# Optimization experiments

Hardware: AMD Instinct MI355X
Metric: run time of the kernel (lower is better)

## Reference

```python
import jax, jax.numpy as jnp
import numpy as np

SIZE = 4096       # reservoir width
STEPS = 512       # num_steps
BETA = 1.0        # leak factor (LSMNeuron default beta=1.0)
THRESHOLD = 10.0  # LSMNeuron threshold=10

# Heaviside spike with atan surrogate gradient (snntorch default surrogate)
@jax.custom_vjp
def heaviside(x):
    return (x > 0).astype(x.dtype)

def _h_fwd(x):
    return (x > 0).astype(x.dtype), x

def _h_bwd(x, g):
    # snntorch ATan surrogate with alpha=2: d/dx = 1 / (1 + (pi*x)^2)
    return (g / (1.0 + (jnp.pi * x) ** 2),)

heaviside.defvjp(_h_fwd, _h_bwd)


def setup_inputs() -> dict:
    key = jax.random.key(0)
    kx, kw = jax.random.split(key)
    x = jax.random.normal(kx, (STEPS, SIZE), dtype=jnp.float32)
    # fc1 weight: Linear(2*size, size), no bias. Input half | recurrent half.
    W = jax.random.normal(kw, (SIZE, 2 * SIZE), dtype=jnp.float32) / np.sqrt(2 * SIZE)
    return {"x": x, "W": W}


def reference(x, W):
    # Split weight: Wx acts on the external input, Ws on recurrent spikes.
    Wx = W[:, :SIZE]   # [size, size]
    Ws = W[:, SIZE:]   # [size, size]
    # Precompute the input-driven current for all steps as one big GEMM.
    cur_x = jnp.einsum('ts,os->to', x, Wx)  # [steps, size]

    def step(carry, cur_xt):
        spk, mem = carry
        cur = cur_xt + Ws @ spk            # fc1(concat(x[t], spk))
        mem = BETA * mem + cur             # leaky integrate
        spk = heaviside(mem - THRESHOLD)   # fire
        mem = mem - spk * THRESHOLD        # subtract reset
        return (spk, mem), (spk, mem)

    init = (jnp.zeros((SIZE,), jnp.float32), jnp.zeros((SIZE,), jnp.float32))
    _, (spk_rec, mem_rec) = jax.lax.scan(step, init, cur_x)
    # original detaches spk_rec
    return jax.lax.stop_gradient(spk_rec), mem_rec
```

## Files before the change

kernel.cpp:

```cpp
#include <hip/hip_runtime.h>
#include <stdint.h>

#define N_SIZE 4096
#define N_STEPS 512
#define WROW 8192
#define THRESH 10.0f
#define CCAP 12

#define WST_BYTES ((size_t)(N_SIZE + 1) * N_SIZE * 4)
#define SMEM_OFF  WST_BYTES
#define SLST_OFF  (WST_BYTES + (size_t)N_SIZE * 4)
#define FULL_WS   (SLST_OFF + (size_t)(N_SIZE + 17) * 4)

#define F4E(v, j) ((j) == 0 ? (v).x : (j) == 1 ? (v).y : (j) == 2 ? (v).z : (v).w)
#define ADD4(a, b) { (a).x += (b).x; (a).y += (b).y; (a).z += (b).z; (a).w += (b).w; }

__global__ __launch_bounds__(256) void k_transpose(const float* __restrict__ W,
                                                   float* __restrict__ WsT) {
    __shared__ float tile[32][33];
    const int bs = blockIdx.x * 32;
    const int bo = blockIdx.y * 32;
    const int tx = threadIdx.x;
    const int ty = threadIdx.y;
#pragma unroll
    for (int j = 0; j < 4; ++j)
        tile[ty + j * 8][tx] = W[(size_t)(bo + ty + j * 8) * WROW + N_SIZE + bs + tx];
    __syncthreads();
#pragma unroll
    for (int j = 0; j < 4; ++j)
        WsT[(size_t)(bs + ty + j * 8) * N_SIZE + bo + tx] = tile[tx][ty + j * 8];
}

__global__ __launch_bounds__(256) void k_zero_row(float* __restrict__ WsT) {
    WsT[(size_t)N_SIZE * N_SIZE + blockIdx.x * 256 + threadIdx.x] = 0.f;
}

#define BM 64
#define BN 128
#define BK 16
#define KHALF (N_SIZE / 2)
#define ALD 68
#define BLD 132

__global__ __launch_bounds__(128) void k_gemm(const float* __restrict__ x,
                                              const float* __restrict__ W,
                                              float* __restrict__ dst0,
                                              float* __restrict__ dst1) {
    __shared__ float As[BK][ALD];
    __shared__ float Bs[BK][BLD];
    const int tid = threadIdx.x;
    const int bm = blockIdx.y * BM;
    const int bn = blockIdx.x * BN;
    const int kb0 = blockIdx.z * KHALF;
    float* dst = blockIdx.z ? dst1 : dst0;

    const int m0 = (tid >> 4) << 3;
    const int n0 = (tid & 15) << 2;
    const int ar = tid >> 2;
    const int ac = (tid & 3) << 2;
    const float* Ap = &x[(size_t)(bm + ar) * N_SIZE + kb0 + ac];
    const float* Bp = &W[(size_t)(bn + ar) * WROW + kb0 + ac];

    float4 pa0 = *(const float4*)&Ap[0];
    float4 pa1 = *(const float4*)&Ap[(size_t)32 * N_SIZE];
    float4 pb0 = *(const float4*)&Bp[0];
    float4 pb1 = *(const float4*)&Bp[(size_t)32 * WROW];
    float4 pb2 = *(const float4*)&Bp[(size_t)64 * WROW];
    float4 pb3 = *(const float4*)&Bp[(size_t)96 * WROW];

    float acc[8][8];
#pragma unroll
    for (int i = 0; i < 8; ++i)
#pragma unroll
        for (int j = 0; j < 8; ++j) acc[i][j] = 0.f;

    const int nkt = KHALF / BK;
    for (int kt = 0; kt < nkt; ++kt) {
        __syncthreads();
#pragma unroll
        for (int j = 0; j < 4; ++j) {
            As[ac + j][ar]      = F4E(pa0, j);
            As[ac + j][ar + 32] = F4E(pa1, j);
            Bs[ac + j][ar]      = F4E(pb0, j);
            Bs[ac + j][ar + 32] = F4E(pb1, j);
            Bs[ac + j][ar + 64] = F4E(pb2, j);
            Bs[ac + j][ar + 96] = F4E(pb3, j);
        }
        __syncthreads();
        if (kt + 1 < nkt) {
            const float* Ap2 = Ap + (size_t)(kt + 1) * BK;
            const float* Bp2 = Bp + (size_t)(kt + 1) * BK;
            pa0 = *(const float4*)&Ap2[0];
            pa1 = *(const float4*)&Ap2[(size_t)32 * N_SIZE];
            pb0 = *(const float4*)&Bp2[0];
            pb1 = *(const float4*)&Bp2[(size_t)32 * WROW];
            pb2 = *(const float4*)&Bp2[(size_t)64 * WROW];
            pb3 = *(const float4*)&Bp2[(size_t)96 * WROW];
        }
#pragma unroll
        for (int k = 0; k < BK; ++k) {
            const float4 a0 = *(const float4*)&As[k][m0];
            const float4 a1 = *(const float4*)&As[k][m0 + 4];
            const float4 b0 = *(const float4*)&Bs[k][n0];
            const float4 b1 = *(const float4*)&Bs[k][n0 + 64];
            const float av[8] = {a0.x, a0.y, a0.z, a0.w, a1.x, a1.y, a1.z, a1.w};
            const float bv[8] = {b0.x, b0.y, b0.z, b0.w, b1.x, b1.y, b1.z, b1.w};
#pragma unroll
            for (int i = 0; i < 8; ++i)
#pragma unroll
                for (int j = 0; j < 8; ++j)
                    acc[i][j] = fmaf(av[i], bv[j], acc[i][j]);
        }
    }
#pragma unroll
    for (int i = 0; i < 8; ++i) {
        float* cp = &dst[(size_t)(bm + m0 + i) * N_SIZE + bn];
        const float4 o0 = {acc[i][0], acc[i][1], acc[i][2], acc[i][3]};
        const float4 o1 = {acc[i][4], acc[i][5], acc[i][6], acc[i][7]};
        *(float4*)&cp[n0] = o0;
        *(float4*)&cp[n0 + 64] = o1;
    }
}

__global__ __launch_bounds__(256) void k_reduce(float* __restrict__ acc,
                                                const float* __restrict__ part) {
    const size_t i = ((size_t)blockIdx.x * 256 + threadIdx.x) * 4;
    const float4 a = *(const float4*)&acc[i];
    const float4 b = *(const float4*)&part[i];
    const float4 r = {a.x + b.x, a.y + b.y, a.z + b.z, a.w + b.w};
    *(float4*)&acc[i] = r;
}

#define GCOL(k)                                                               \
    const int s##k = __builtin_amdgcn_readfirstlane(lst[n0 + k]);             \
    const float* p##k = &WsT[(size_t)s##k * N_SIZE + base];

__global__ __launch_bounds__(512) void k_scanF(const float* __restrict__ WsT,
                                               float* __restrict__ spk_out,
                                               float* __restrict__ mem_out,
                                               float* __restrict__ smem,
                                               int* __restrict__ slst,
                                               int t0, int t1) {
    __shared__ int lst[N_SIZE + 16];
    __shared__ int wcnt[8];
    const int tid = threadIdx.x;
    const int wave = tid >> 6;
    const int lane = tid & 63;
    const int base = tid << 3;
    const unsigned long long below = (lane == 0) ? 0ULL : (~0ULL >> (64 - lane));

    float4 m0 = {0.f, 0.f, 0.f, 0.f}, m1 = {0.f, 0.f, 0.f, 0.f};
    int tot = 0;

    if (t0 != 0) {
        m0 = *(const float4*)&smem[base];
        m1 = *(const float4*)&smem[base + 4];
        for (int i = tid; i < N_SIZE + 16; i += 512) lst[i] = slst[i];
        tot = slst[N_SIZE + 16];
        __syncthreads();
    }

    float4 cn0 = *(const float4*)&mem_out[(size_t)t0 * N_SIZE + base];
    float4 cn1 = *(const float4*)&mem_out[(size_t)t0 * N_SIZE + base + 4];

    for (int t = t0; t < t1; ++t) {
        float4 c0 = cn0, c1 = cn1;

        for (int n0 = 0; n0 < tot; n0 += CCAP) {
            GCOL(0)  GCOL(1)  GCOL(2)  GCOL(3)  GCOL(4)  GCOL(5)
            GCOL(6)  GCOL(7)  GCOL(8)  GCOL(9)  GCOL(10) GCOL(11)
            const float4 a0 = *(const float4*)&p0[0],  b0v = *(const float4*)&p0[4];
            const float4 a1 = *(const float4*)&p1[0],  b1v = *(const float4*)&p1[4];
            const float4 a2 = *(const float4*)&p2[0],  b2v = *(const float4*)&p2[4];
            const float4 a3 = *(const float4*)&p3[0],  b3v = *(const float4*)&p3[4];
            const float4 a4 = *(const float4*)&p4[0],  b4v = *(const float4*)&p4[4];
            const float4 a5 = *(const float4*)&p5[0],  b5v = *(const float4*)&p5[4];
            const float4 a6 = *(const float4*)&p6[0],  b6v = *(const float4*)&p6[4];
            const float4 a7 = *(const float4*)&p7[0],  b7v = *(const float4*)&p7[4];
            const float4 a8 = *(const float4*)&p8[0],  b8v = *(const float4*)&p8[4];
            const float4 a9 = *(const float4*)&p9[0],  b9v = *(const float4*)&p9[4];
            const float4 aA = *(const float4*)&p10[0], bAv = *(const float4*)&p10[4];
            const float4 aB = *(const float4*)&p11[0], bBv = *(const float4*)&p11[4];
            ADD4(c0, a0) ADD4(c1, b0v)
            ADD4(c0, a1) ADD4(c1, b1v)
            ADD4(c0, a2) ADD4(c1, b2v)
            ADD4(c0, a3) ADD4(c1, b3v)
            ADD4(c0, a4) ADD4(c1, b4v)
            ADD4(c0, a5) ADD4(c1, b5v)
            ADD4(c0, a6) ADD4(c1, b6v)
            ADD4(c0, a7) ADD4(c1, b7v)
            ADD4(c0, a8) ADD4(c1, b8v)
            ADD4(c0, a9) ADD4(c1, b9v)
            ADD4(c0, aA) ADD4(c1, bAv)
            ADD4(c0, aB) ADD4(c1, bBv)
        }

        ADD4(m0, c0) ADD4(m1, c1)
        const bool s0b = m0.x > THRESH, s1b = m0.y > THRESH;
        const bool s2b = m0.z > THRESH, s3b = m0.w > THRESH;
        const bool s4b = m1.x > THRESH, s5b = m1.y > THRESH;
        const bool s6b = m1.z > THRESH, s7b = m1.w > THRESH;
        m0.x -= s0b ? THRESH : 0.f;  m0.y -= s1b ? THRESH : 0.f;
        m0.z -= s2b ? THRESH : 0.f;  m0.w -= s3b ? THRESH : 0.f;
        m1.x -= s4b ? THRESH : 0.f;  m1.y -= s5b ? THRESH : 0.f;
        m1.z -= s6b ? THRESH : 0.f;  m1.w -= s7b ? THRESH : 0.f;

        const unsigned long long B0 = __ballot(s0b), B1 = __ballot(s1b);
        const unsigned long long B2 = __ballot(s2b), B3 = __ballot(s3b);
        const unsigned long long B4 = __ballot(s4b), B5 = __ballot(s5b);
        const unsigned long long B6 = __ballot(s6b), B7 = __ballot(s7b);
        const int pre = __popcll(B0 & below) + __popcll(B1 & below) +
                        __popcll(B2 & below) + __popcll(B3 & below) +
                        __popcll(B4 & below) + __popcll(B5 & below) +
                        __popcll(B6 & below) + __popcll(B7 & below);
        if (lane == 0)
            wcnt[wave] = __popcll(B0) + __popcll(B1) + __popcll(B2) + __popcll(B3) +
                         __popcll(B4) + __popcll(B5) + __popcll(B6) + __popcll(B7);

        const float4 sp0 = {s0b ? 1.f : 0.f, s1b ? 1.f : 0.f,
                            s2b ? 1.f : 0.f, s3b ? 1.f : 0.f};
        const float4 sp1 = {s4b ? 1.f : 0.f, s5b ? 1.f : 0.f,
                            s6b ? 1.f : 0.f, s7b ? 1.f : 0.f};
        float* srow = &spk_out[(size_t)t * N_SIZE + base];
        float* mrow = &mem_out[(size_t)t * N_SIZE + base];
        *(float4*)&srow[0] = sp0;
        *(float4*)&srow[4] = sp1;
        *(float4*)&mrow[0] = m0;
        *(float4*)&mrow[4] = m1;
        const int tn = (t + 1 < N_STEPS) ? (t + 1) : t;
        cn0 = *(const float4*)&mem_out[(size_t)tn * N_SIZE + base];
        cn1 = *(const float4*)&mem_out[(size_t)tn * N_SIZE + base + 4];

        __syncthreads();

        int woff = 0, tt = 0;
#pragma unroll
        for (int w = 0; w < 8; ++w) {
            const int cw = wcnt[w];
            if (w < wave) woff += cw;
            tt += cw;
        }
        int off = woff + pre;
        if (s0b) lst[off++] = base + 0;
        if (s1b) lst[off++] = base + 1;
        if (s2b) lst[off++] = base + 2;
        if (s3b) lst[off++] = base + 3;
        if (s4b) lst[off++] = base + 4;
        if (s5b) lst[off++] = base + 5;
        if (s6b) lst[off++] = base + 6;
        if (s7b) lst[off++] = base + 7;
        if (tid < 16) lst[tt + tid] = N_SIZE;
        __syncthreads();

        tot = tt;
    }

    if (t1 < N_STEPS) {
        *(float4*)&smem[base] = m0;
        *(float4*)&smem[base + 4] = m1;
        for (int i = tid; i < N_SIZE + 16; i += 512) slst[i] = lst[i];
        if (tid == 0) slst[N_SIZE + 16] = tot;
    }
}

template <int USE_WST>
__global__ __launch_bounds__(1024) void k_scan1(const float* __restrict__ WsT,
                                                const float* __restrict__ W,
                                                float* __restrict__ spk_out,
                                                float* __restrict__ mem_out) {
    __shared__ int lists[2][N_SIZE];
    __shared__ int wcnt[16];
    const int tid = threadIdx.x;
    const int wave = tid >> 6;
    const int lane = tid & 63;
    const int base = tid << 2;
    const unsigned long long below = (lane == 0) ? 0ULL : (~0ULL >> (64 - lane));

    float4 mem = {0.f, 0.f, 0.f, 0.f};
    int cnt = 0, cur = 0;
    for (int t = 0; t < N_STEPS; ++t) {
        float* mrow = &mem_out[(size_t)t * N_SIZE + base];
        float4 c = *(const float4*)mrow;
        const int* lstp = lists[cur];
        for (int i = 0; i < cnt; ++i) {
            const int s = lstp[i];
            float4 w0;
            if (USE_WST) {
                w0 = *(const float4*)&WsT[(size_t)s * N_SIZE + base];
            } else {
                w0.x = W[(size_t)(base + 0) * WROW + N_SIZE + s];
                w0.y = W[(size_t)(base + 1) * WROW + N_SIZE + s];
                w0.z = W[(size_t)(base + 2) * WROW + N_SIZE + s];
                w0.w = W[(size_t)(base + 3) * WROW + N_SIZE + s];
            }
            ADD4(c, w0)
        }
        ADD4(mem, c)
        const bool s0 = mem.x > THRESH, s1 = mem.y > THRESH;
        const bool s2 = mem.z > THRESH, s3 = mem.w > THRESH;
        mem.x -= s0 ? THRESH : 0.f;  mem.y -= s1 ? THRESH : 0.f;
        mem.z -= s2 ? THRESH : 0.f;  mem.w -= s3 ? THRESH : 0.f;
        const float4 spkv = {s0 ? 1.f : 0.f, s1 ? 1.f : 0.f,
                             s2 ? 1.f : 0.f, s3 ? 1.f : 0.f};
        *(float4*)&spk_out[(size_t)t * N_SIZE + base] = spkv;
        *(float4*)mrow = mem;
        const unsigned long long b0 = __ballot(s0), b1 = __ballot(s1);
        const unsigned long long b2 = __ballot(s2), b3 = __ballot(s3);
        const int pre = __popcll(b0 & below) + __popcll(b1 & below) +
                        __popcll(b2 & below) + __popcll(b3 & below);
        if (lane == 0)
            wcnt[wave] = __popcll(b0) + __popcll(b1) + __popcll(b2) + __popcll(b3);
        __syncthreads();
        int woff = 0, total = 0;
#pragma unroll
        for (int wv = 0; wv < 16; ++wv) {
            const int cw = wcnt[wv];
            if (wv < wave) woff += cw;
            total += cw;
        }
        int* nxt = lists[cur ^ 1];
        int off = woff + pre;
        if (s0) nxt[off++] = base;
        if (s1) nxt[off++] = base + 1;
        if (s2) nxt[off++] = base + 2;
        if (s3) nxt[off++] = base + 3;
        __syncthreads();
        cnt = total;
        cur ^= 1;
    }
}

extern "C" void kernel_launch(void* const* d_in, const int* in_sizes, int n_in,
                              void* d_out, int out_size, void* d_ws, size_t ws_size,
                              hipStream_t stream) {
    const float* x = (const float*)d_in[0];
    const float* W = (const float*)d_in[1];
    float* spk_out = (float*)d_out;
    float* mem_out = spk_out + (size_t)N_STEPS * N_SIZE;
    float* WsT = (float*)d_ws;
    float* smem = (float*)((char*)d_ws + SMEM_OFF);
    int* slst = (int*)((char*)d_ws + SLST_OFF);
    const bool full = ws_size >= FULL_WS;
    const bool use_wst = ws_size >= (size_t)N_SIZE * N_SIZE * 4;

    if (full) {
        k_zero_row<<<16, 256, 0, stream>>>(WsT);
        k_transpose<<<dim3(N_SIZE / 32, N_SIZE / 32), dim3(32, 8), 0, stream>>>(W, WsT);
    } else if (use_wst) {
        k_transpose<<<dim3(N_SIZE / 32, N_SIZE / 32), dim3(32, 8), 0, stream>>>(W, WsT);
    }

    k_gemm<<<dim3(N_SIZE / BN, N_STEPS / BM, 2), 128, 0, stream>>>(x, W, mem_out, spk_out);
    k_reduce<<<(N_STEPS * N_SIZE) / (256 * 4), 256, 0, stream>>>(mem_out, spk_out);

    if (full) {
        k_scanF<<<1, 512, 0, stream>>>(WsT, spk_out, mem_out, smem, slst, 0, 256);
        k_scanF<<<1, 512, 0, stream>>>(WsT, spk_out, mem_out, smem, slst, 256, 512);
    } else if (use_wst) {
        k_scan1<1><<<1, 1024, 0, stream>>>(WsT, W, spk_out, mem_out);
    } else {
        k_scan1<0><<<1, 1024, 0, stream>>>(WsT, W, spk_out, mem_out);
    }
}
```

Baseline: 1.811 ms.

## Replace split scan with single 256-thread scan using 16 neurons per thread

Measured after the change: 2.346 ms. 29.5% more time.

```diff
diff --git a/kernel.cpp b/kernel.cpp
--- a/kernel.cpp
+++ b/kernel.cpp
@@ -5,12 +5,8 @@
 #define N_STEPS 512
 #define WROW 8192
 #define THRESH 10.0f
-#define CCAP 12
 
 #define WST_BYTES ((size_t)(N_SIZE + 1) * N_SIZE * 4)
-#define SMEM_OFF  WST_BYTES
-#define SLST_OFF  (WST_BYTES + (size_t)N_SIZE * 4)
-#define FULL_WS   (SLST_OFF + (size_t)(N_SIZE + 17) * 4)
 
 #define F4E(v, j) ((j) == 0 ? (v).x : (j) == 1 ? (v).y : (j) == 2 ? (v).z : (v).w)
 #define ADD4(a, b) { (a).x += (b).x; (a).y += (b).y; (a).z += (b).z; (a).w += (b).w; }
@@ -131,135 +127,110 @@
     *(float4*)&acc[i] = r;
 }
 
-#define GCOL(k)                                                               \
-    const int s##k = __builtin_amdgcn_readfirstlane(lst[n0 + k]);             \
-    const float* p##k = &WsT[(size_t)s##k * N_SIZE + base];
-
-__global__ __launch_bounds__(512) void k_scanF(const float* __restrict__ WsT,
-                                               float* __restrict__ spk_out,
-                                               float* __restrict__ mem_out,
-                                               float* __restrict__ smem,
-                                               int* __restrict__ slst,
-                                               int t0, int t1) {
-    __shared__ int lst[N_SIZE + 16];
-    __shared__ int wcnt[8];
+__global__ __launch_bounds__(256, 1) void k_scanR(const float* __restrict__ WsT,
+                                                  float* __restrict__ spk_out,
+                                                  float* __restrict__ mem_out) {
+    __shared__ int lst[2][N_SIZE + 8];
+    __shared__ int wcnt[4];
     const int tid = threadIdx.x;
     const int wave = tid >> 6;
     const int lane = tid & 63;
-    const int base = tid << 3;
+    const int base = tid << 4;
     const unsigned long long below = (lane == 0) ? 0ULL : (~0ULL >> (64 - lane));
 
-    float4 m0 = {0.f, 0.f, 0.f, 0.f}, m1 = {0.f, 0.f, 0.f, 0.f};
-    int tot = 0;
-
-    if (t0 != 0) {
-        m0 = *(const float4*)&smem[base];
-        m1 = *(const float4*)&smem[base + 4];
-        for (int i = tid; i < N_SIZE + 16; i += 512) lst[i] = slst[i];
-        tot = slst[N_SIZE + 16];
-        __syncthreads();
-    }
-
-    float4 cn0 = *(const float4*)&mem_out[(size_t)t0 * N_SIZE + base];
-    float4 cn1 = *(const float4*)&mem_out[(size_t)t0 * N_SIZE + base + 4];
-
-    for (int t = t0; t < t1; ++t) {
-        float4 c0 = cn0, c1 = cn1;
-
-        for (int n0 = 0; n0 < tot; n0 += CCAP) {
-            GCOL(0)  GCOL(1)  GCOL(2)  GCOL(3)  GCOL(4)  GCOL(5)
-            GCOL(6)  GCOL(7)  GCOL(8)  GCOL(9)  GCOL(10) GCOL(11)
-            const float4 a0 = *(const float4*)&p0[0],  b0v = *(const float4*)&p0[4];
-            const float4 a1 = *(const float4*)&p1[0],  b1v = *(const float4*)&p1[4];
-            const float4 a2 = *(const float4*)&p2[0],  b2v = *(const float4*)&p2[4];
-            const float4 a3 = *(const float4*)&p3[0],  b3v = *(const float4*)&p3[4];
-            const float4 a4 = *(const float4*)&p4[0],  b4v = *(const float4*)&p4[4];
-            const float4 a5 = *(const float4*)&p5[0],  b5v = *(const float4*)&p5[4];
-            const float4 a6 = *(const float4*)&p6[0],  b6v = *(const float4*)&p6[4];
-            const float4 a7 = *(const float4*)&p7[0],  b7v = *(const float4*)&p7[4];
-            const float4 a8 = *(const float4*)&p8[0],  b8v = *(const float4*)&p8[4];
-            const float4 a9 = *(const float4*)&p9[0],  b9v = *(const float4*)&p9[4];
-            const float4 aA = *(const float4*)&p10[0], bAv = *(const float4*)&p10[4];
-            const float4 aB = *(const float4*)&p11[0], bBv = *(const float4*)&p11[4];
-            ADD4(c0, a0) ADD4(c1, b0v)
-            ADD4(c0, a1) ADD4(c1, b1v)
-            ADD4(c0, a2) ADD4(c1, b2v)
-            ADD4(c0, a3) ADD4(c1, b3v)
-            ADD4(c0, a4) ADD4(c1, b4v)
-            ADD4(c0, a5) ADD4(c1, b5v)
-            ADD4(c0, a6) ADD4(c1, b6v)
-            ADD4(c0, a7) ADD4(c1, b7v)
-            ADD4(c0, a8) ADD4(c1, b8v)
-            ADD4(c0, a9) ADD4(c1, b9v)
-            ADD4(c0, aA) ADD4(c1, bAv)
-            ADD4(c0, aB) ADD4(c1, bBv)
-        }
-
-        ADD4(m0, c0) ADD4(m1, c1)
-        const bool s0b = m0.x > THRESH, s1b = m0.y > THRESH;
-        const bool s2b = m0.z > THRESH, s3b = m0.w > THRESH;
-        const bool s4b = m1.x > THRESH, s5b = m1.y > THRESH;
-        const bool s6b = m1.z > THRESH, s7b = m1.w > THRESH;
-        m0.x -= s0b ? THRESH : 0.f;  m0.y -= s1b ? THRESH : 0.f;
-        m0.z -= s2b ? THRESH : 0.f;  m0.w -= s3b ? THRESH : 0.f;
-        m1.x -= s4b ? THRESH : 0.f;  m1.y -= s5b ? THRESH : 0.f;
-        m1.z -= s6b ? THRESH : 0.f;  m1.w -= s7b ? THRESH : 0.f;
-
-        const unsigned long long B0 = __ballot(s0b), B1 = __ballot(s1b);
-        const unsigned long long B2 = __ballot(s2b), B3 = __ballot(s3b);
-        const unsigned long long B4 = __ballot(s4b), B5 = __ballot(s5b);
-        const unsigned long long B6 = __ballot(s6b), B7 = __ballot(s7b);
-        const int pre = __popcll(B0 & below) + __popcll(B1 & below) +
-                        __popcll(B2 & below) + __popcll(B3 & below) +
-                        __popcll(B4 & below) + __popcll(B5 & below) +
-                        __popcll(B6 & below) + __popcll(B7 & below);
-        if (lane == 0)
-            wcnt[wave] = __popcll(B0) + __popcll(B1) + __popcll(B2) + __popcll(B3) +
-                         __popcll(B4) + __popcll(B5) + __popcll(B6) + __popcll(B7);
-
-        const float4 sp0 = {s0b ? 1.f : 0.f, s1b ? 1.f : 0.f,
-                            s2b ? 1.f : 0.f, s3b ? 1.f : 0.f};
-        const float4 sp1 = {s4b ? 1.f : 0.f, s5b ? 1.f : 0.f,
-                            s6b ? 1.f : 0.f, s7b ? 1.f : 0.f};
+    float4 mem[4];
+#pragma unroll
+    for (int q = 0; q < 4; ++q) mem[q] = {0.f, 0.f, 0.f, 0.f};
+    int tot = 0, buf = 0;
+
+    float4 cn[4];
+#pragma unroll
+    for (int q = 0; q < 4; ++q)
+        cn[q] = *(const float4*)&mem_out[base + q * 4];
+
+    for (int t = 0; t < N_STEPS; ++t) {
+        float4 c[4];
+#pragma unroll
+        for (int q = 0; q < 4; ++q) c[q] = cn[q];
+
+        const int tn = (t + 1 < N_STEPS) ? (t + 1) : t;
+        const float* nr = &mem_out[(size_t)tn * N_SIZE + base];
+#pragma unroll
+        for (int q = 0; q < 4; ++q) cn[q] = *(const float4*)&nr[q * 4];
+
+        const int* lp = lst[buf];
+        for (int i0 = 0; i0 < tot; i0 += 8) {
+            const float* pp[8];
+#pragma unroll
+            for (int j = 0; j < 8; ++j) {
+                const int s = __builtin_amdgcn_readfirstlane(lp[i0 + j]);
+                pp[j] = &WsT[(size_t)s * N_SIZE + base];
+            }
+            float4 v[8][4];
+#pragma unroll
+            for (int j = 0; j < 8; ++j)
+#pragma unroll
+                for (int q = 0; q < 4; ++q)
+                    v[j][q] = *(const float4*)&pp[j][q * 4];
+#pragma unroll
+            for (int j = 0; j < 8; ++j)
+#pragma unroll
+                for (int q = 0; q < 4; ++q)
+                    ADD4(c[q], v[j][q])
+        }
+
+        bool sb[16];
+#pragma unroll
+        for (int q = 0; q < 4; ++q) {
+            ADD4(mem[q], c[q])
+            sb[q * 4 + 0] = mem[q].x > THRESH;
+            sb[q * 4 + 1] = mem[q].y > THRESH;
+            sb[q * 4 + 2] = mem[q].z > THRESH;
+            sb[q * 4 + 3] = mem[q].w > THRESH;
+            mem[q].x -= sb[q * 4 + 0] ? THRESH : 0.f;
+            mem[q].y -= sb[q * 4 + 1] ? THRESH : 0.f;
+            mem[q].z -= sb[q * 4 + 2] ? THRESH : 0.f;
+            mem[q].w -= sb[q * 4 + 3] ? THRESH : 0.f;
+        }
+
+        int pre = 0, wtot = 0;
+#pragma unroll
+        for (int j = 0; j < 16; ++j) {
+            const unsigned long long B = __ballot(sb[j]);
+            pre += __popcll(B & below);
+            wtot += __popcll(B);
+        }
+        if (lane == 0) wcnt[wave] = wtot;
+
         float* srow = &spk_out[(size_t)t * N_SIZE + base];
         float* mrow = &mem_out[(size_t)t * N_SIZE + base];
-        *(float4*)&srow[0] = sp0;
-        *(float4*)&srow[4] = sp1;
-        *(float4*)&mrow[0] = m0;
-        *(float4*)&mrow[4] = m1;
-        const int tn = (t + 1 < N_STEPS) ? (t + 1) : t;
-        cn0 = *(const float4*)&mem_out[(size_t)tn * N_SIZE + base];
-        cn1 = *(const float4*)&mem_out[(size_t)tn * N_SIZE + base + 4];
+#pragma unroll
+        for (int q = 0; q < 4; ++q) {
+            const float4 sp = {sb[q * 4 + 0] ? 1.f : 0.f, sb[q * 4 + 1] ? 1.f : 0.f,
+                               sb[q * 4 + 2] ? 1.f : 0.f, sb[q * 4 + 3] ? 1.f : 0.f};
+            *(float4*)&srow[q * 4] = sp;
+            *(float4*)&mrow[q * 4] = mem[q];
+        }
 
         __syncthreads();
 
         int woff = 0, tt = 0;
 #pragma unroll
-        for (int w = 0; w < 8; ++w) {
+        for (int w = 0; w < 4; ++w) {
             const int cw = wcnt[w];
             if (w < wave) woff += cw;
             tt += cw;
         }
+        int* nxt = lst[buf ^ 1];
         int off = woff + pre;
-        if (s0b) lst[off++] = base + 0;
-        if (s1b) lst[off++] = base + 1;
-        if (s2b) lst[off++] = base + 2;
-        if (s3b) lst[off++] = base + 3;
-        if (s4b) lst[off++] = base + 4;
-        if (s5b) lst[off++] = base + 5;
-        if (s6b) lst[off++] = base + 6;
-        if (s7b) lst[off++] = base + 7;
-        if (tid < 16) lst[tt + tid] = N_SIZE;
+#pragma unroll
+        for (int j = 0; j < 16; ++j)
+            if (sb[j]) nxt[off++] = base + j;
+        if (tid < 8) nxt[tt + tid] = N_SIZE;
         __syncthreads();
 
         tot = tt;
-    }
-
-    if (t1 < N_STEPS) {
-        *(float4*)&smem[base] = m0;
-        *(float4*)&smem[base + 4] = m1;
-        for (int i = tid; i < N_SIZE + 16; i += 512) slst[i] = lst[i];
-        if (tid == 0) slst[N_SIZE + 16] = tot;
+        buf ^= 1;
     }
 }
 
@@ -338,9 +309,7 @@
     float* spk_out = (float*)d_out;
     float* mem_out = spk_out + (size_t)N_STEPS * N_SIZE;
     float* WsT = (float*)d_ws;
-    float* smem = (float*)((char*)d_ws + SMEM_OFF);
-    int* slst = (int*)((char*)d_ws + SLST_OFF);
-    const bool full = ws_size >= FULL_WS;
+    const bool full = ws_size >= WST_BYTES;
     const bool use_wst = ws_size >= (size_t)N_SIZE * N_SIZE * 4;
 
     if (full) {
@@ -354,8 +323,7 @@
     k_reduce<<<(N_STEPS * N_SIZE) / (256 * 4), 256, 0, stream>>>(mem_out, spk_out);
 
     if (full) {
-        k_scanF<<<1, 512, 0, stream>>>(WsT, spk_out, mem_out, smem, slst, 0, 256);
-        k_scanF<<<1, 512, 0, stream>>>(WsT, spk_out, mem_out, smem, slst, 256, 512);
+        k_scanR<<<1, 256, 0, stream>>>(WsT, spk_out, mem_out);
     } else if (use_wst) {
         k_scan1<1><<<1, 1024, 0, stream>>>(WsT, W, spk_out, mem_out);
     } else {
```
